# Optimization experiments

Measured on AMD Instinct MI355X. Metric: run time of the kernel, lower is better.

Reference implementation:

```python
import jax, jax.numpy as jnp
import numpy as np
import math

B, T, D_MOTION = 2, 1536, 256
D_MODEL, N_HEADS, D_FF, N_LAYERS = 512, 8, 2048, 6
D_HEAD = D_MODEL // N_HEADS
FPS = 30
PERIOD = FPS // 2
CONTEXT_FRAMES = 10
NEG = -1e9  # large negative instead of -inf so fully-masked rows give uniform attn, not NaN


def _w(k, shape, fan_in):
    return jax.random.normal(k, shape, jnp.float32) / np.sqrt(fan_in)


def setup_inputs() -> dict:
    key = jax.random.key(0)
    ks = jax.random.split(key, 16)
    L = N_LAYERS
    din = D_MOTION + 5 + 1
    inp = {
        'motion': jax.random.normal(ks[0], (B, T, D_MOTION), jnp.float32),
        'traj': jax.random.normal(ks[1], (B, T, 5), jnp.float32),
        'me_w1': _w(ks[2], (din, D_MODEL), din), 'me_b1': jnp.zeros((D_MODEL,), jnp.float32),
        'me_w2': _w(ks[3], (D_MODEL, D_MODEL), D_MODEL), 'me_b2': jnp.zeros((D_MODEL,), jnp.float32),
        'wq': _w(ks[4], (L, D_MODEL, D_MODEL), D_MODEL), 'bq': jnp.zeros((L, D_MODEL), jnp.float32),
        'wk': _w(ks[5], (L, D_MODEL, D_MODEL), D_MODEL), 'bk': jnp.zeros((L, D_MODEL), jnp.float32),
        'wv': _w(ks[6], (L, D_MODEL, D_MODEL), D_MODEL), 'bv': jnp.zeros((L, D_MODEL), jnp.float32),
        'wo': _w(ks[7], (L, D_MODEL, D_MODEL), D_MODEL), 'bo': jnp.zeros((L, D_MODEL), jnp.float32),
        'ln1_g': jnp.ones((L, D_MODEL), jnp.float32), 'ln1_b': jnp.zeros((L, D_MODEL), jnp.float32),
        'ffn_w1': _w(ks[8], (L, D_MODEL, D_FF), D_MODEL), 'ffn_b1': jnp.zeros((L, D_FF), jnp.float32),
        'ffn_w2': _w(ks[9], (L, D_FF, D_MODEL), D_FF), 'ffn_b2': jnp.zeros((L, D_MODEL), jnp.float32),
        'ln2_g': jnp.ones((L, D_MODEL), jnp.float32), 'ln2_b': jnp.zeros((L, D_MODEL), jnp.float32),
        'fln_g': jnp.ones((D_MODEL,), jnp.float32), 'fln_b': jnp.zeros((D_MODEL,), jnp.float32),
        'dec_w1': _w(ks[10], (D_MODEL, D_MODEL), D_MODEL), 'dec_b1': jnp.zeros((D_MODEL,), jnp.float32),
        'dec_w2': _w(ks[11], (D_MODEL, D_MOTION), D_MODEL), 'dec_b2': jnp.zeros((D_MOTION,), jnp.float32),
    }
    return inp


def _layer_norm(x, g, b):
    m = jnp.mean(x, axis=-1, keepdims=True)
    v = jnp.mean((x - m) ** 2, axis=-1, keepdims=True)
    return (x - m) * jax.lax.rsqrt(v + 1e-5) * g + b


def _leaky(x):
    return jnp.where(x >= 0, x, 0.01 * x)


def _forward(motion, traj, me_w1, me_b1, me_w2, me_b2, wq, bq, wk, bk, wv, bv, wo, bo,
             ln1_g, ln1_b, ffn_w1, ffn_b1, ffn_w2, ffn_b2, ln2_g, ln2_b,
             fln_g, fln_b, dec_w1, dec_b1, dec_w2, dec_b2):
    idx = jnp.arange(T)
    dist = jnp.abs(idx[:, None] - idx[None, :])                       # [T,T]
    atten_bias = -(dist // PERIOD).astype(jnp.float32)                # periodic distance bias

    # context mask: keep first context_frames and last frame
    batch_mask = jnp.ones((T, 1), jnp.float32).at[CONTEXT_FRAMES:-1].set(0.0)
    mask = jnp.broadcast_to(batch_mask[None], (B, T, 1))              # [B,T,1]
    cf = jnp.ones((T,), bool).at[CONTEXT_FRAMES:-1].set(False)        # constrained frames

    original_motion = motion
    motion = motion * mask

    # motion encoder (dropout inactive at eval)
    h = jnp.concatenate([motion, traj, mask], axis=-1)                # [B,T,D_MOTION+6]
    x = _leaky(h @ me_w1 + me_b1)
    x = _leaky(x @ me_w2 + me_b2)

    # periodic positional embedding (sinusoidal on pos mod period)
    pos = jnp.mod(jnp.arange(T, dtype=jnp.float32), float(PERIOD))
    half = D_MODEL // 2
    div = jnp.exp(-np.log(10000.0) * (2.0 * jnp.arange(half, dtype=jnp.float32)) / D_MODEL)
    ang = pos[:, None] * div[None, :]
    pe = jnp.concatenate([jnp.sin(ang), jnp.cos(ang)], axis=-1)       # [T,D_MODEL]
    x = x + pe[None]

    # dynamically growing attention window
    num_trans = T - CONTEXT_FRAMES - 1
    ksz = math.ceil(num_trans / 2 / N_LAYERS) * 2 + 1
    kern = jnp.ones((ksz,), jnp.float32)
    thr = ksz // 2
    scale = 1.0 / np.sqrt(D_HEAD)

    for i in range(N_LAYERS):
        # attn mask: True = blocked
        amask = (dist > thr) | (~cf)[None, :]                         # [T,T]
        h = _layer_norm(x, ln1_g[i], ln1_b[i])                        # pre-layernorm
        q = (h @ wq[i] + bq[i]).reshape(B, T, N_HEADS, D_HEAD)
        k = (h @ wk[i] + bk[i]).reshape(B, T, N_HEADS, D_HEAD)
        v = (h @ wv[i] + bv[i]).reshape(B, T, N_HEADS, D_HEAD)
        scores = jnp.einsum('bqhd,bkhd->bhqk', q, k) * scale + atten_bias
        scores = jnp.where(amask[None, None], NEG, scores)
        attn = jax.nn.softmax(scores, axis=-1)
        out = jnp.einsum('bhqk,bkhd->bqhd', attn, v).reshape(B, T, D_MODEL)
        x = x + out @ wo[i] + bo[i]
        # position-wise FFN (pre-layernorm)
        h = _layer_norm(x, ln2_g[i], ln2_b[i])
        x = x + jax.nn.relu(h @ ffn_w1[i] + ffn_b1[i]) @ ffn_w2[i] + ffn_b2[i]
        # grow constrained frames by conv1d with ones kernel (same padding)
        cf = jnp.convolve(cf.astype(jnp.float32), kern, mode='same') > 0.5

    x = _layer_norm(x, fln_g, fln_b)
    x = _leaky(x @ dec_w1 + dec_b1)
    x = x @ dec_w2 + dec_b2                                           # [B,T,D_MOTION]
    out = original_motion * mask + x * (1.0 - mask)
    return out, mask


def reference(motion, traj, me_w1, me_b1, me_w2, me_b2, wq, bq, wk, bk, wv, bv, wo, bo,
              ln1_g, ln1_b, ffn_w1, ffn_b1, ffn_w2, ffn_b2, ln2_g, ln2_b,
              fln_g, fln_b, dec_w1, dec_b1, dec_w2, dec_b2):
    return _forward(motion, traj, me_w1, me_b1, me_w2, me_b2, wq, bq, wk, bk, wv, bv, wo, bo,
                    ln1_g, ln1_b, ffn_w1, ffn_b1, ffn_w2, ffn_b2, ln2_g, ln2_b,
                    fln_g, fln_b, dec_w1, dec_b1, dec_w2, dec_b2)
```

## Files before the change

### kernel.cpp

```cpp
#include <hip/hip_runtime.h>
#include <math.h>

typedef unsigned short ushort_t;
typedef unsigned int uint_t;
typedef __bf16 bf16x4 __attribute__((ext_vector_type(4)));
typedef __bf16 bf16x8 __attribute__((ext_vector_type(8)));
typedef float f32x4 __attribute__((ext_vector_type(4)));

#define T_SEQ   1536
#define NB      2
#define MROWS   3072
#define DMODEL  512
#define NHEADS  8
#define DHEAD   64
#define DFF     2048
#define DMOTION 256
#define NLAYERS 6
#define PERIODN 15
#define CTXF    10
#define THRW    128
#define KIN     384

__device__ __forceinline__ float bf2f(ushort_t u) { return __uint_as_float((uint_t)u << 16); }
__device__ __forceinline__ ushort_t f2bf(float f) {
    uint_t x = __float_as_uint(f);
    return (ushort_t)((x + 0x7fffu + ((x >> 16) & 1u)) >> 16);
}

__device__ __forceinline__ void gl2lds(const ushort_t* g, ushort_t* l) {
    __builtin_amdgcn_global_load_lds((const __attribute__((address_space(1))) void*)g,
                                     (__attribute__((address_space(3))) void*)l, 16, 0, 0);
}

__global__ __launch_bounds__(256) void pe_k(float* __restrict__ pe) {
    int idx = blockIdx.x * 256 + threadIdx.x;
    if (idx >= PERIODN * DMODEL) return;
    int p = idx / DMODEL, c = idx % DMODEL;
    int j = (c < DMODEL / 2) ? c : (c - DMODEL / 2);
    float div = __expf(-logf(10000.0f) * (2.0f * (float)j) / (float)DMODEL);
    float ang = (float)p * div;
    pe[idx] = (c < DMODEL / 2) ? sinf(ang) : cosf(ang);
}

__global__ __launch_bounds__(256) void build_k(const float* __restrict__ motion,
                                               const float* __restrict__ traj,
                                               ushort_t* __restrict__ hin,
                                               float* __restrict__ mask_out) {
    int idx = blockIdx.x * 256 + threadIdx.x;
    if (idx >= MROWS * KIN) return;
    int row = idx / KIN, c = idx % KIN;
    int t = row % T_SEQ;
    float mv = (t < CTXF || t == T_SEQ - 1) ? 1.0f : 0.0f;
    float val;
    if (c < DMOTION)            val = motion[(size_t)row * DMOTION + c] * mv;
    else if (c < DMOTION + 5)   val = traj[(size_t)row * 5 + (c - DMOTION)];
    else if (c == DMOTION + 5)  val = mv;
    else                        val = 0.0f;
    hin[idx] = f2bf(val);
    if (c == 0) mask_out[row] = mv;
}

__global__ __launch_bounds__(256)
void tconv_k(const float* __restrict__ src, size_t sstride,
             ushort_t* __restrict__ dst, size_t dstride,
             int K, int N, int Kpad) {
    __shared__ float t[32][33];
    src += (size_t)blockIdx.z * sstride;
    dst += (size_t)blockIdx.z * dstride;
    const int kb = blockIdx.y * 32, nb = blockIdx.x * 32;
    const int tx = threadIdx.x & 31, ty = threadIdx.x >> 5;
#pragma unroll
    for (int i = 0; i < 4; ++i) {
        int k = kb + ty + i * 8, n = nb + tx;
        t[ty + i * 8][tx] = (k < K && n < N) ? src[(size_t)k * N + n] : 0.0f;
    }
    __syncthreads();
#pragma unroll
    for (int i = 0; i < 4; ++i) {
        int n = nb + ty + i * 8, kk = kb + tx;
        if (n < N && kk < Kpad) dst[(size_t)n * Kpad + kk] = f2bf(t[tx][ty + i * 8]);
    }
}

__global__ __launch_bounds__(256)
void tconv_qkv_k(const float* __restrict__ wq, const float* __restrict__ wk,
                 const float* __restrict__ wv, ushort_t* __restrict__ qkvt) {
    __shared__ float t[32][33];
    const int z = blockIdx.z, s = z % 3, l = z / 3;
    const float* src = (s == 0 ? wq : s == 1 ? wk : wv) + (size_t)l * DMODEL * DMODEL;
    ushort_t* dst = qkvt + (size_t)z * DMODEL * DMODEL;
    const int kb = blockIdx.y * 32, nb = blockIdx.x * 32;
    const int tx = threadIdx.x & 31, ty = threadIdx.x >> 5;
#pragma unroll
    for (int i = 0; i < 4; ++i)
        t[ty + i * 8][tx] = src[(size_t)(kb + ty + i * 8) * DMODEL + nb + tx];
    __syncthreads();
#pragma unroll
    for (int i = 0; i < 4; ++i)
        dst[(size_t)(nb + ty + i * 8) * DMODEL + kb + tx] = f2bf(t[tx][ty + i * 8]);
}

__global__ __launch_bounds__(256)
void bcat_k(const float* __restrict__ bq, const float* __restrict__ bk,
            const float* __restrict__ bv, float* __restrict__ bqkv) {
    int idx = blockIdx.x * 256 + threadIdx.x;
    if (idx >= NLAYERS * 3 * DMODEL) return;
    int l = idx / (3 * DMODEL), n = idx % (3 * DMODEL);
    int s = n >> 9, c = n & 511;
    const float* b = (s == 0 ? bq : s == 1 ? bk : bv);
    bqkv[idx] = b[l * DMODEL + c];
}

#define CL  68
template <int ACT, bool RES, bool PE, bool OUTBF>
__global__ __launch_bounds__(256)
void qgemm_k(const ushort_t* __restrict__ A, int K,
             const ushort_t* __restrict__ Wt,
             const float* __restrict__ bias,
             const float* __restrict__ res,
             const float* __restrict__ pe15,
             void* __restrict__ Cout, int N) {
    __shared__ ushort_t smem[2][(32 + 64) * 128];
    const int tid = threadIdx.x;
    const int lane = tid & 63, wid = tid >> 6;
    const int m0 = blockIdx.y * 32, n0 = blockIdx.x * 64;
    const int l4 = lane >> 4, l15 = lane & 15;
    const int lrow = lane >> 4;
    const int lu   = lane & 15;

    f32x4 acc[2][4];
#pragma unroll
    for (int m = 0; m < 2; ++m)
#pragma unroll
        for (int n = 0; n < 4; ++n) acc[m][n] = (f32x4){0.f, 0.f, 0.f, 0.f};

    const int niter = K >> 7;

    auto stage = [&](int buf, int k0) {
        ushort_t* dst = &smem[buf][0];
#pragma unroll
        for (int j = 0; j < 6; ++j) {
            const int inst = wid * 6 + j;
            if (inst < 8) {
                const int row = inst * 4 + lrow;
                const int u = lu ^ (row & 15);
                gl2lds(A + (size_t)(m0 + row) * K + k0 + u * 8, dst + inst * 512);
            } else {
                const int bi = inst - 8;
                const int row = bi * 4 + lrow;
                const int u = lu ^ (row & 15);
                gl2lds(Wt + (size_t)(n0 + row) * K + k0 + u * 8,
                       dst + 32 * 128 + bi * 512);
            }
        }
    };

    const int kbyte = wid * 64;
    auto rdfrag = [&](const ushort_t* t, int row) -> bf16x8 {
        const int off0 = kbyte + l4 * 8;
        const int off1 = kbyte + 32 + l4 * 8;
        const int a0 = row * 256 + (((off0 & ~15) ^ ((row & 15) << 4)) | (off0 & 15));
        const int a1 = row * 256 + (((off1 & ~15) ^ ((row & 15) << 4)) | (off1 & 15));
        bf16x4 lo = *(const bf16x4*)((const char*)t + a0);
        bf16x4 hi = *(const bf16x4*)((const char*)t + a1);
        return __builtin_shufflevector(lo, hi, 0, 1, 2, 3, 4, 5, 6, 7);
    };

    stage(0, 0);
    __syncthreads();
    int cur = 0;
    for (int t = 0; t < niter; ++t) {
        if (t + 1 < niter) stage(cur ^ 1, (t + 1) << 7);
        const ushort_t* As = &smem[cur][0];
        const ushort_t* Bs = &smem[cur][32 * 128];
        bf16x8 af[2], bf[4];
#pragma unroll
        for (int m = 0; m < 2; ++m) af[m] = rdfrag(As, m * 16 + l15);
#pragma unroll
        for (int n = 0; n < 4; ++n) bf[n] = rdfrag(Bs, n * 16 + l15);
#pragma unroll
        for (int m = 0; m < 2; ++m)
#pragma unroll
            for (int n = 0; n < 4; ++n)
                acc[m][n] = __builtin_amdgcn_mfma_f32_16x16x32_bf16(af[m], bf[n], acc[m][n], 0, 0, 0);
        __syncthreads();
        cur ^= 1;
    }

    float* cb0 = (float*)&smem[0][0];
    float* cb1 = (float*)&smem[1][0];
    if (wid >= 2) {
        float* cb = (wid == 2) ? cb0 : cb1;
#pragma unroll
        for (int m = 0; m < 2; ++m)
#pragma unroll
            for (int n = 0; n < 4; ++n)
#pragma unroll
                for (int r = 0; r < 4; ++r)
                    cb[(m * 16 + l4 * 4 + r) * CL + n * 16 + l15] = acc[m][n][r];
    }
    __syncthreads();
    if (wid < 2) {
        float* cb = (wid == 0) ? cb0 : cb1;
#pragma unroll
        for (int m = 0; m < 2; ++m)
#pragma unroll
            for (int n = 0; n < 4; ++n)
#pragma unroll
                for (int r = 0; r < 4; ++r)
                    cb[(m * 16 + l4 * 4 + r) * CL + n * 16 + l15] += acc[m][n][r];
    }
    __syncthreads();

    const int row = tid >> 3, c0 = (tid & 7) * 8;
    const int grow = m0 + row;
#pragma unroll
    for (int j = 0; j < 8; ++j) {
        const int gcol = n0 + c0 + j;
        float v = cb0[row * CL + c0 + j] + cb1[row * CL + c0 + j] + bias[gcol];
        if (ACT == 1) v = v >= 0.f ? v : 0.01f * v;
        else if (ACT == 2) v = fmaxf(v, 0.f);
        if (PE) v += pe15[((grow % T_SEQ) % PERIODN) * DMODEL + gcol];
        if (RES) v += res[(size_t)grow * N + gcol];
        if (OUTBF) ((ushort_t*)Cout)[(size_t)grow * N + gcol] = f2bf(v);
        else       ((float*)Cout)[(size_t)grow * N + gcol] = v;
    }
}

__global__ __launch_bounds__(256)
void ln_k(const float* __restrict__ X, const float* __restrict__ g,
          const float* __restrict__ b, ushort_t* __restrict__ Y) {
    const int wid = threadIdx.x >> 6, lane = threadIdx.x & 63;
    const int row = blockIdx.x * 4 + wid;
    const float* x = X + (size_t)row * DMODEL;
    float v[8], s = 0.f;
#pragma unroll
    for (int j = 0; j < 8; ++j) { v[j] = x[lane + 64 * j]; s += v[j]; }
#pragma unroll
    for (int o = 32; o; o >>= 1) s += __shfl_xor(s, o);
    const float mean = s * (1.0f / DMODEL);
    float vs = 0.f;
#pragma unroll
    for (int j = 0; j < 8; ++j) { float d = v[j] - mean; vs += d * d; }
#pragma unroll
    for (int o = 32; o; o >>= 1) vs += __shfl_xor(vs, o);
    const float inv = rsqrtf(vs * (1.0f / DMODEL) + 1e-5f);
    ushort_t* y = Y + (size_t)row * DMODEL;
#pragma unroll
    for (int j = 0; j < 8; ++j) {
        const int c = lane + 64 * j;
        y[c] = f2bf((v[j] - mean) * inv * g[c] + b[c]);
    }
}

__global__ __launch_bounds__(1024)
void vmeanp_k(const ushort_t* __restrict__ qkv, float* __restrict__ vmp) {
    __shared__ float red[16][64];
    const int bh = blockIdx.x, ch = blockIdx.y;
    const int b = bh >> 3, h = bh & 7;
    const int wid = threadIdx.x >> 6, lane = threadIdx.x & 63;
    const ushort_t* Vb = qkv + (size_t)(b * T_SEQ) * 1536 + 1024 + h * 64 + lane;
    float s = 0.f;
    const int t0 = ch * 192;
    for (int t = t0 + wid; t < t0 + 192; t += 16) s += bf2f(Vb[(size_t)t * 1536]);
    red[wid][lane] = s;
    __syncthreads();
    if (wid == 0) {
        float tot = 0.f;
#pragma unroll
        for (int i = 0; i < 16; ++i) tot += red[i][lane];
        vmp[(ch * 16 + bh) * 64 + lane] = tot;
    }
}

__global__ __launch_bounds__(1024)
void vmred_k(const float* __restrict__ vmp, float* __restrict__ vm) {
    const int t = threadIdx.x;
    float s = 0.f;
#pragma unroll
    for (int ch = 0; ch < 8; ++ch) s += vmp[ch * 1024 + t];
    vm[t] = s * (1.0f / T_SEQ);
}

__global__ __launch_bounds__(256)
void vfill_k(const float* __restrict__ vm, ushort_t* __restrict__ attout, int q0) {
    const int qrow = q0 + blockIdx.x, b = blockIdx.y;
    const int tid = threadIdx.x;
#pragma unroll
    for (int r = 0; r < 2; ++r) {
        const int c = tid + r * 256;
        attout[(size_t)(b * T_SEQ + qrow) * DMODEL + c] = f2bf(vm[b * 512 + c]);
    }
}

#define KLD 72
#define VLD 36
__global__ __launch_bounds__(256)
void attn3_k(const ushort_t* __restrict__ qkv, ushort_t* __restrict__ attout,
             int lo, int hi, int nlow, int qhi0, int tl, int st) {
    __shared__ ushort_t klds_[4][32 * KLD];
    __shared__ ushort_t vlds_[4][64 * VLD];
    const int lane = threadIdx.x & 63, wid = threadIdx.x >> 6;
    const int s = blockIdx.x * 4 + wid;
    if (s >= st) return;
    const int h = blockIdx.y, b = blockIdx.z;
    const int l15 = lane & 15, l4 = lane >> 4;

    int qb, qend;
    if (s < tl) { qb = 16 * s;                qend = nlow - 1; }
    else        { qb = qhi0 + 16 * (s - tl);  qend = T_SEQ - 1; }
    const int nr = qend - qb;

    ushort_t* klds = klds_[wid];
    ushort_t* vlds = vlds_[wid];
    const size_t rbase = (size_t)(b * T_SEQ) * 1536;
    const int q = qb + l15;

    const int qrow_r = min(q, T_SEQ - 1);
    const ushort_t* qptr = qkv + rbase + (size_t)qrow_r * 1536 + h * 64;
    bf16x8 bq[2];
#pragma unroll
    for (int kh = 0; kh < 2; ++kh) {
        bf16x4 lo4 = *(const bf16x4*)(qptr + kh * 32 + l4 * 4);
        bf16x4 hi4 = *(const bf16x4*)(qptr + kh * 32 + 16 + l4 * 4);
        bq[kh] = __builtin_shufflevector(lo4, hi4, 0, 1, 2, 3, 4, 5, 6, 7);
    }

    const int band0 = max(0, qb - THRW);
    const int band1 = min(T_SEQ - 1, qb + 15 + THRW);
    const int i1s = band0, i1e = min(band1, lo - 1);
    const int i2s = max(band0, hi), i2e = band1;

    f32x4 O[4] = {{0.f,0.f,0.f,0.f},{0.f,0.f,0.f,0.f},{0.f,0.f,0.f,0.f},{0.f,0.f,0.f,0.f}};
    float m = -3.0e38f, lsum = 0.f;

#pragma unroll 1
    for (int seg = 0; seg < 2; ++seg) {
        const int s0 = seg ? i2s : i1s, s1 = seg ? i2e : i1e;
#pragma unroll 1
        for (int c0 = s0; c0 <= s1; c0 += 32) {
#pragma unroll
            for (int i = 0; i < 4; ++i) {
                const int idx = i * 64 + lane;
                const int row = idx >> 3, c = (idx & 7) * 8;
                const int kr = min(c0 + row, T_SEQ - 1);
                const uint4 kv = *(const uint4*)(qkv + rbase + (size_t)kr * 1536 + 512 + h * 64 + c);
                *(uint4*)&klds[row * KLD + c] = kv;
                const uint4 vv = *(const uint4*)(qkv + rbase + (size_t)kr * 1536 + 1024 + h * 64 + c);
                const ushort_t* vp = (const ushort_t*)&vv;
#pragma unroll
                for (int d = 0; d < 8; ++d) vlds[(c + d) * VLD + row] = vp[d];
            }
            f32x4 sacc[2];
#pragma unroll
            for (int ks = 0; ks < 2; ++ks) {
                f32x4 a = {0.f, 0.f, 0.f, 0.f};
#pragma unroll
                for (int kh = 0; kh < 2; ++kh) {
                    const ushort_t* kp = &klds[(16 * ks + l15) * KLD + kh * 32];
                    bf16x4 lo4 = *(const bf16x4*)(kp + l4 * 4);
                    bf16x4 hi4 = *(const bf16x4*)(kp + 16 + l4 * 4);
                    bf16x8 ak = __builtin_shufflevector(lo4, hi4, 0, 1, 2, 3, 4, 5, 6, 7);
                    a = __builtin_amdgcn_mfma_f32_16x16x32_bf16(ak, bq[kh], a, 0, 0, 0);
                }
                sacc[ks] = a;
            }
            float sv[8];
            bool vld[8];
            float cm = -3.0e38f;
#pragma unroll
            for (int ks = 0; ks < 2; ++ks)
#pragma unroll
                for (int r = 0; r < 4; ++r) {
                    const int key = c0 + 16 * ks + 4 * l4 + r;
                    const int dist = (q > key) ? (q - key) : (key - q);
                    const bool v = (dist <= THRW) && (key < lo || key >= hi) && (key < T_SEQ);
                    const int ii = ks * 4 + r;
                    sv[ii] = sacc[ks][r] * 0.125f - (float)(dist / PERIODN);
                    vld[ii] = v;
                    cm = fmaxf(cm, v ? sv[ii] : -3.0e38f);
                }
            cm = fmaxf(cm, __shfl_xor(cm, 16));
            cm = fmaxf(cm, __shfl_xor(cm, 32));
            const float mnew = fmaxf(m, cm);
            const float sc = __expf(m - mnew);
            m = mnew;
            float p[8], psum = 0.f;
#pragma unroll
            for (int ii = 0; ii < 8; ++ii) {
                p[ii] = vld[ii] ? __expf(sv[ii] - mnew) : 0.f;
                psum += p[ii];
            }
            psum += __shfl_xor(psum, 16);
            psum += __shfl_xor(psum, 32);
            lsum = lsum * sc + psum;
#pragma unroll
            for (int ds = 0; ds < 4; ++ds) O[ds] *= sc;
            bf16x8 pb;
#pragma unroll
            for (int ii = 0; ii < 8; ++ii) pb[ii] = (__bf16)p[ii];
#pragma unroll
            for (int ds = 0; ds < 4; ++ds) {
                const ushort_t* vp2 = &vlds[(16 * ds + l15) * VLD];
                bf16x4 lo4 = *(const bf16x4*)(vp2 + 4 * l4);
                bf16x4 hi4 = *(const bf16x4*)(vp2 + 16 + 4 * l4);
                bf16x8 av = __builtin_shufflevector(lo4, hi4, 0, 1, 2, 3, 4, 5, 6, 7);
                O[ds] = __builtin_amdgcn_mfma_f32_16x16x32_bf16(av, pb, O[ds], 0, 0, 0);
            }
        }
    }
    if (l15 <= nr) {
        const float inv = 1.0f / lsum;
        ushort_t* op = attout + (size_t)(b * T_SEQ + qb + l15) * DMODEL + h * 64;
#pragma unroll
        for (int ds = 0; ds < 4; ++ds)
#pragma unroll
            for (int r = 0; r < 4; ++r)
                op[16 * ds + 4 * l4 + r] = f2bf(O[ds][r] * inv);
    }
}

__global__ __launch_bounds__(256)
void final_k(const float* __restrict__ motion, const float* __restrict__ xdec,
             float* __restrict__ out) {
    int idx = blockIdx.x * 256 + threadIdx.x;
    if (idx >= MROWS * DMOTION) return;
    const int row = idx >> 8;
    const int t = row % T_SEQ;
    const float mv = (t < CTXF || t == T_SEQ - 1) ? 1.0f : 0.0f;
    out[idx] = motion[idx] * mv + xdec[idx] * (1.0f - mv);
}

extern "C" void kernel_launch(void* const* d_in, const int* in_sizes, int n_in,
                              void* d_out, int out_size, void* d_ws, size_t ws_size,
                              hipStream_t stream) {
    const float* motion = (const float*)d_in[0];
    const float* traj   = (const float*)d_in[1];
    const float* me_w1  = (const float*)d_in[2];
    const float* me_b1  = (const float*)d_in[3];
    const float* me_w2  = (const float*)d_in[4];
    const float* me_b2  = (const float*)d_in[5];
    const float* wq = (const float*)d_in[6];
    const float* bq = (const float*)d_in[7];
    const float* wk = (const float*)d_in[8];
    const float* bk = (const float*)d_in[9];
    const float* wv = (const float*)d_in[10];
    const float* bv = (const float*)d_in[11];
    const float* wo = (const float*)d_in[12];
    const float* bo = (const float*)d_in[13];
    const float* ln1_g = (const float*)d_in[14];
    const float* ln1_b = (const float*)d_in[15];
    const float* ffn_w1 = (const float*)d_in[16];
    const float* ffn_b1 = (const float*)d_in[17];
    const float* ffn_w2 = (const float*)d_in[18];
    const float* ffn_b2 = (const float*)d_in[19];
    const float* ln2_g = (const float*)d_in[20];
    const float* ln2_b = (const float*)d_in[21];
    const float* fln_g = (const float*)d_in[22];
    const float* fln_b = (const float*)d_in[23];
    const float* dec_w1 = (const float*)d_in[24];
    const float* dec_b1 = (const float*)d_in[25];
    const float* dec_w2 = (const float*)d_in[26];
    const float* dec_b2 = (const float*)d_in[27];

    float* out = (float*)d_out;
    float* mask_out = out + (size_t)MROWS * DMOTION;

    char* base = (char*)d_ws;
    auto alloc = [&](size_t bytes) { char* p = base; base += (bytes + 255) & ~(size_t)255; return p; };

    ushort_t* qkvt  = (ushort_t*)alloc((size_t)NLAYERS * 1536 * 512 * 2);
    ushort_t* wot   = (ushort_t*)alloc((size_t)NLAYERS * 512 * 512 * 2);
    ushort_t* ffn1t = (ushort_t*)alloc((size_t)NLAYERS * 2048 * 512 * 2);
    ushort_t* ffn2t = (ushort_t*)alloc((size_t)NLAYERS * 512 * 2048 * 2);
    ushort_t* mew1t = (ushort_t*)alloc((size_t)512 * KIN * 2);
    ushort_t* mew2t = (ushort_t*)alloc((size_t)512 * 512 * 2);
    ushort_t* dec1t = (ushort_t*)alloc((size_t)512 * 512 * 2);
    ushort_t* dec2t = (ushort_t*)alloc((size_t)256 * 512 * 2);
    float*    bqkv  = (float*)alloc((size_t)NLAYERS * 1536 * 4);
    float*    pe15  = (float*)alloc((size_t)PERIODN * DMODEL * 4);
    float*    vmp   = (float*)alloc((size_t)8 * 16 * 64 * 4);
    float*    vm    = (float*)alloc((size_t)16 * 64 * 4);
    ushort_t* hin   = (ushort_t*)alloc((size_t)MROWS * KIN * 2);
    float*    x     = (float*)alloc((size_t)MROWS * DMODEL * 4);
    ushort_t* h     = (ushort_t*)alloc((size_t)MROWS * DMODEL * 2);
    ushort_t* qkv   = (ushort_t*)alloc((size_t)MROWS * 1536 * 2);
    ushort_t* ff    = (ushort_t*)alloc((size_t)MROWS * DFF * 2);
    float*    xdec  = (float*)qkv;

    const dim3 blk(256);
    pe_k<<<(PERIODN * DMODEL + 255) / 256, blk, 0, stream>>>(pe15);
    build_k<<<(MROWS * KIN + 255) / 256, blk, 0, stream>>>(motion, traj, hin, mask_out);

    tconv_qkv_k<<<dim3(16, 16, 18), blk, 0, stream>>>(wq, wk, wv, qkvt);
    tconv_k<<<dim3(16, 16, 6), blk, 0, stream>>>(wo, 512 * 512, wot, 512 * 512, 512, 512, 512);
    tconv_k<<<dim3(64, 16, 6), blk, 0, stream>>>(ffn_w1, 512 * 2048, ffn1t, 2048 * 512, 512, 2048, 512);
    tconv_k<<<dim3(16, 64, 6), blk, 0, stream>>>(ffn_w2, 2048 * 512, ffn2t, 512 * 2048, 2048, 512, 2048);
    tconv_k<<<dim3(16, 12, 1), blk, 0, stream>>>(me_w1, 0, mew1t, 0, 262, 512, KIN);
    tconv_k<<<dim3(16, 16, 1), blk, 0, stream>>>(me_w2, 0, mew2t, 0, 512, 512, 512);
    tconv_k<<<dim3(16, 16, 1), blk, 0, stream>>>(dec_w1, 0, dec1t, 0, 512, 512, 512);
    tconv_k<<<dim3(8, 16, 1),  blk, 0, stream>>>(dec_w2, 0, dec2t, 0, 512, 256, 512);
    bcat_k<<<(NLAYERS * 1536 + 255) / 256, blk, 0, stream>>>(bq, bk, bv, bqkv);

    const dim3 gs512(8, 96), gs1536(24, 96), gsff(32, 96), gs256(4, 96);

    qgemm_k<1, false, false, true ><<<gs512, blk, 0, stream>>>(hin, KIN, mew1t, me_b1, nullptr, nullptr, h, 512);
    qgemm_k<1, false, true,  false><<<gs512, blk, 0, stream>>>(h, 512, mew2t, me_b2, nullptr, pe15, x, 512);

    for (int i = 0; i < NLAYERS; ++i) {
        const int lo = CTXF + THRW * i;
        const int hi = (T_SEQ - 1) - THRW * i;
        int qlow_end = lo + 127;
        int qhi0 = hi - 128;
        int nlow, ninact;
        if (qhi0 <= qlow_end + 1) {
            nlow = T_SEQ; qhi0 = T_SEQ; ninact = 0;
        } else {
            nlow = qlow_end + 1;
            ninact = qhi0 - nlow;
        }
        const int tl2 = (nlow + 15) / 16;
        const int th2 = (T_SEQ - qhi0 + 15) / 16;
        const int st  = tl2 + th2;

        ln_k<<<MROWS / 4, blk, 0, stream>>>(x, ln1_g + i * 512, ln1_b + i * 512, h);
        qgemm_k<0, false, false, true><<<gs1536, blk, 0, stream>>>(h, 512, qkvt + (size_t)i * 1536 * 512, bqkv + i * 1536, nullptr, nullptr, qkv, 1536);
        if (ninact > 0) {
            vmeanp_k<<<dim3(16, 8), dim3(1024), 0, stream>>>(qkv, vmp);
            vmred_k<<<1, dim3(1024), 0, stream>>>(vmp, vm);
            vfill_k<<<dim3(ninact, NB), blk, 0, stream>>>(vm, h, nlow);
        }
        attn3_k<<<dim3((st + 3) / 4, NHEADS, NB), blk, 0, stream>>>(qkv, h, lo, hi, nlow, qhi0, tl2, st);
        qgemm_k<0, true, false, false><<<gs512, blk, 0, stream>>>(h, 512, wot + (size_t)i * 512 * 512, bo + i * 512, x, nullptr, x, 512);
        ln_k<<<MROWS / 4, blk, 0, stream>>>(x, ln2_g + i * 512, ln2_b + i * 512, h);
        qgemm_k<2, false, false, true><<<gsff, blk, 0, stream>>>(h, 512, ffn1t + (size_t)i * 2048 * 512, ffn_b1 + i * 2048, nullptr, nullptr, ff, 2048);
        qgemm_k<0, true, false, false><<<gs512, blk, 0, stream>>>(ff, 2048, ffn2t + (size_t)i * 512 * 2048, ffn_b2 + i * 512, x, nullptr, x, 512);
    }

    ln_k<<<MROWS / 4, blk, 0, stream>>>(x, fln_g, fln_b, h);
    qgemm_k<1, false, false, true ><<<gs512, blk, 0, stream>>>(h, 512, dec1t, dec_b1, nullptr, nullptr, ff, 512);
    qgemm_k<0, false, false, false><<<gs256, blk, 0, stream>>>(ff, 512, dec2t, dec_b2, nullptr, nullptr, xdec, 256);

    final_k<<<(MROWS * DMOTION + 255) / 256, blk, 0, stream>>>(motion, xdec, out);
}
```

Before: 813.4 us.

## Fuse mask blend into decoder GEMM, compute V-mean from LN output, merge fill into attention

The final mask blend is folded into the last decoder GEMM epilogue (new ACT==3), which removes final_k and the xdec round trip. The V mean for inactive rows is now computed as mean(h)·Wv + bv from the layernorm output via vsum_k and vdot_k, and the fill of inactive rows moves into spare waves of the attention kernel, replacing the separate vmred and vfill launches. MFMA sections in attention are wrapped with s_setprio to raise wave priority. The result is fewer launches and less strided reading, but the V-mean path now relies on linearity, which changes its rounding relative to the bf16 V values.

```diff
diff --git a/kernel.cpp b/kernel.cpp
--- a/kernel.cpp
+++ b/kernel.cpp
@@ -220,6 +220,11 @@
         float v = cb0[row * CL + c0 + j] + cb1[row * CL + c0 + j] + bias[gcol];
         if (ACT == 1) v = v >= 0.f ? v : 0.01f * v;
         else if (ACT == 2) v = fmaxf(v, 0.f);
+        else if (ACT == 3) {
+            const int t2 = grow % T_SEQ;
+            const float mv = (t2 < CTXF || t2 == T_SEQ - 1) ? 1.0f : 0.0f;
+            v = res[(size_t)grow * N + gcol] * mv + v * (1.0f - mv);
+        }
         if (PE) v += pe15[((grow % T_SEQ) % PERIODN) * DMODEL + gcol];
         if (RES) v += res[(size_t)grow * N + gcol];
         if (OUTBF) ((ushort_t*)Cout)[(size_t)grow * N + gcol] = f2bf(v);
@@ -254,56 +259,68 @@
 }
 
 __global__ __launch_bounds__(1024)
-void vmeanp_k(const ushort_t* __restrict__ qkv, float* __restrict__ vmp) {
-    __shared__ float red[16][64];
-    const int bh = blockIdx.x, ch = blockIdx.y;
-    const int b = bh >> 3, h = bh & 7;
-    const int wid = threadIdx.x >> 6, lane = threadIdx.x & 63;
-    const ushort_t* Vb = qkv + (size_t)(b * T_SEQ) * 1536 + 1024 + h * 64 + lane;
+void vsum_k(const ushort_t* __restrict__ h, float* __restrict__ hp) {
+    __shared__ float red[1024];
+    const int b = blockIdx.x, ch = blockIdx.y;
+    const int c = threadIdx.x & 511, half = threadIdx.x >> 9;
+    const ushort_t* hb = h + (size_t)(b * T_SEQ + ch * 192) * DMODEL + c;
     float s = 0.f;
-    const int t0 = ch * 192;
-    for (int t = t0 + wid; t < t0 + 192; t += 16) s += bf2f(Vb[(size_t)t * 1536]);
-    red[wid][lane] = s;
-    __syncthreads();
-    if (wid == 0) {
-        float tot = 0.f;
-#pragma unroll
-        for (int i = 0; i < 16; ++i) tot += red[i][lane];
-        vmp[(ch * 16 + bh) * 64 + lane] = tot;
-    }
-}
-
-__global__ __launch_bounds__(1024)
-void vmred_k(const float* __restrict__ vmp, float* __restrict__ vm) {
+    for (int r = half; r < 192; r += 2) s += bf2f(hb[(size_t)r * DMODEL]);
+    red[threadIdx.x] = s;
+    __syncthreads();
+    if (threadIdx.x < 512)
+        hp[(b * 8 + ch) * 512 + threadIdx.x] = red[threadIdx.x] + red[threadIdx.x + 512];
+}
+
+__global__ __launch_bounds__(256)
+void vdot_k(const float* __restrict__ hp, const ushort_t* __restrict__ wvt,
+            const float* __restrict__ bv, float* __restrict__ vm) {
+    __shared__ float mh[512];
+    __shared__ float red[256];
+    const int b = blockIdx.x, seg = blockIdx.y;
     const int t = threadIdx.x;
+    for (int c = t; c < 512; c += 256) {
+        float s = 0.f;
+#pragma unroll
+        for (int ch = 0; ch < 8; ++ch) s += hp[(b * 8 + ch) * 512 + c];
+        mh[c] = s * (1.0f / T_SEQ);
+    }
+    __syncthreads();
+    const int col = seg * 128 + (t & 127);
+    const int kh = (t >> 7) * 256;
+    const ushort_t* w = wvt + (size_t)col * 512 + kh;
     float s = 0.f;
-#pragma unroll
-    for (int ch = 0; ch < 8; ++ch) s += vmp[ch * 1024 + t];
-    vm[t] = s * (1.0f / T_SEQ);
-}
-
-__global__ __launch_bounds__(256)
-void vfill_k(const float* __restrict__ vm, ushort_t* __restrict__ attout, int q0) {
-    const int qrow = q0 + blockIdx.x, b = blockIdx.y;
-    const int tid = threadIdx.x;
-#pragma unroll
-    for (int r = 0; r < 2; ++r) {
-        const int c = tid + r * 256;
-        attout[(size_t)(b * T_SEQ + qrow) * DMODEL + c] = f2bf(vm[b * 512 + c]);
-    }
+    for (int k = 0; k < 256; k += 8) {
+        bf16x8 w8 = *(const bf16x8*)(w + k);
+#pragma unroll
+        for (int j = 0; j < 8; ++j) s += mh[kh + k + j] * (float)w8[j];
+    }
+    red[t] = s;
+    __syncthreads();
+    if (t < 128) vm[b * 512 + col] = red[t] + red[t + 128] + bv[col];
 }
 
 #define KLD 72
 #define VLD 36
 __global__ __launch_bounds__(256)
-void attn3_k(const ushort_t* __restrict__ qkv, ushort_t* __restrict__ attout,
-             int lo, int hi, int nlow, int qhi0, int tl, int st) {
+void attn3_k(const ushort_t* __restrict__ qkv, const float* __restrict__ vm,
+             ushort_t* __restrict__ attout,
+             int lo, int hi, int nlow, int qhi0, int tl, int st, int ft) {
     __shared__ ushort_t klds_[4][32 * KLD];
     __shared__ ushort_t vlds_[4][64 * VLD];
     const int lane = threadIdx.x & 63, wid = threadIdx.x >> 6;
     const int s = blockIdx.x * 4 + wid;
-    if (s >= st) return;
     const int h = blockIdx.y, b = blockIdx.z;
+    if (s >= st) {
+        const int f = s - st;
+        if (f >= ft) return;
+        const int r0 = nlow + 16 * f;
+        const int rend = min(16, qhi0 - r0);
+        const ushort_t ov = f2bf(vm[b * 512 + h * 64 + lane]);
+        ushort_t* op = attout + (size_t)(b * T_SEQ + r0) * DMODEL + h * 64 + lane;
+        for (int r = 0; r < rend; ++r) op[(size_t)r * DMODEL] = ov;
+        return;
+    }
     const int l15 = lane & 15, l4 = lane >> 4;
 
     int qb, qend;
@@ -352,6 +369,7 @@
                 for (int d = 0; d < 8; ++d) vlds[(c + d) * VLD + row] = vp[d];
             }
             f32x4 sacc[2];
+            __builtin_amdgcn_s_setprio(1);
 #pragma unroll
             for (int ks = 0; ks < 2; ++ks) {
                 f32x4 a = {0.f, 0.f, 0.f, 0.f};
@@ -365,6 +383,7 @@
                 }
                 sacc[ks] = a;
             }
+            __builtin_amdgcn_s_setprio(0);
             float sv[8];
             bool vld[8];
             float cm = -3.0e38f;
@@ -399,6 +418,7 @@
             bf16x8 pb;
 #pragma unroll
             for (int ii = 0; ii < 8; ++ii) pb[ii] = (__bf16)p[ii];
+            __builtin_amdgcn_s_setprio(1);
 #pragma unroll
             for (int ds = 0; ds < 4; ++ds) {
                 const ushort_t* vp2 = &vlds[(16 * ds + l15) * VLD];
@@ -407,6 +427,7 @@
                 bf16x8 av = __builtin_shufflevector(lo4, hi4, 0, 1, 2, 3, 4, 5, 6, 7);
                 O[ds] = __builtin_amdgcn_mfma_f32_16x16x32_bf16(av, pb, O[ds], 0, 0, 0);
             }
+            __builtin_amdgcn_s_setprio(0);
         }
     }
     if (l15 <= nr) {
@@ -418,17 +439,6 @@
             for (int r = 0; r < 4; ++r)
                 op[16 * ds + 4 * l4 + r] = f2bf(O[ds][r] * inv);
     }
-}
-
-__global__ __launch_bounds__(256)
-void final_k(const float* __restrict__ motion, const float* __restrict__ xdec,
-             float* __restrict__ out) {
-    int idx = blockIdx.x * 256 + threadIdx.x;
-    if (idx >= MROWS * DMOTION) return;
-    const int row = idx >> 8;
-    const int t = row % T_SEQ;
-    const float mv = (t < CTXF || t == T_SEQ - 1) ? 1.0f : 0.0f;
-    out[idx] = motion[idx] * mv + xdec[idx] * (1.0f - mv);
 }
 
 extern "C" void kernel_launch(void* const* d_in, const int* in_sizes, int n_in,
@@ -479,14 +489,13 @@
     ushort_t* dec2t = (ushort_t*)alloc((size_t)256 * 512 * 2);
     float*    bqkv  = (float*)alloc((size_t)NLAYERS * 1536 * 4);
     float*    pe15  = (float*)alloc((size_t)PERIODN * DMODEL * 4);
-    float*    vmp   = (float*)alloc((size_t)8 * 16 * 64 * 4);
-    float*    vm    = (float*)alloc((size_t)16 * 64 * 4);
+    float*    hp    = (float*)alloc((size_t)NB * 8 * 512 * 4);
+    float*    vm    = (float*)alloc((size_t)NB * 512 * 4);
     ushort_t* hin   = (ushort_t*)alloc((size_t)MROWS * KIN * 2);
     float*    x     = (float*)alloc((size_t)MROWS * DMODEL * 4);
     ushort_t* h     = (ushort_t*)alloc((size_t)MROWS * DMODEL * 2);
     ushort_t* qkv   = (ushort_t*)alloc((size_t)MROWS * 1536 * 2);
     ushort_t* ff    = (ushort_t*)alloc((size_t)MROWS * DFF * 2);
-    float*    xdec  = (float*)qkv;
 
     const dim3 blk(256);
     pe_k<<<(PERIODN * DMODEL + 255) / 256, blk, 0, stream>>>(pe15);
@@ -522,15 +531,15 @@
         const int tl2 = (nlow + 15) / 16;
         const int th2 = (T_SEQ - qhi0 + 15) / 16;
         const int st  = tl2 + th2;
+        const int ft  = (ninact + 15) / 16;
 
         ln_k<<<MROWS / 4, blk, 0, stream>>>(x, ln1_g + i * 512, ln1_b + i * 512, h);
         qgemm_k<0, false, false, true><<<gs1536, blk, 0, stream>>>(h, 512, qkvt + (size_t)i * 1536 * 512, bqkv + i * 1536, nullptr, nullptr, qkv, 1536);
         if (ninact > 0) {
-            vmeanp_k<<<dim3(16, 8), dim3(1024), 0, stream>>>(qkv, vmp);
-            vmred_k<<<1, dim3(1024), 0, stream>>>(vmp, vm);
-            vfill_k<<<dim3(ninact, NB), blk, 0, stream>>>(vm, h, nlow);
+            vsum_k<<<dim3(NB, 8), dim3(1024), 0, stream>>>(h, hp);
+            vdot_k<<<dim3(NB, 4), blk, 0, stream>>>(hp, qkvt + (size_t)i * 1536 * 512 + (size_t)1024 * 512, bqkv + i * 1536 + 1024, vm);
         }
-        attn3_k<<<dim3((st + 3) / 4, NHEADS, NB), blk, 0, stream>>>(qkv, h, lo, hi, nlow, qhi0, tl2, st);
+        attn3_k<<<dim3((st + ft + 3) / 4, NHEADS, NB), blk, 0, stream>>>(qkv, vm, h, lo, hi, nlow, qhi0, tl2, st, ft);
         qgemm_k<0, true, false, false><<<gs512, blk, 0, stream>>>(h, 512, wot + (size_t)i * 512 * 512, bo + i * 512, x, nullptr, x, 512);
         ln_k<<<MROWS / 4, blk, 0, stream>>>(x, ln2_g + i * 512, ln2_b + i * 512, h);
         qgemm_k<2, false, false, true><<<gsff, blk, 0, stream>>>(h, 512, ffn1t + (size_t)i * 2048 * 512, ffn_b1 + i * 2048, nullptr, nullptr, ff, 2048);
@@ -539,7 +548,5 @@
 
     ln_k<<<MROWS / 4, blk, 0, stream>>>(x, fln_g, fln_b, h);
     qgemm_k<1, false, false, true ><<<gs512, blk, 0, stream>>>(h, 512, dec1t, dec_b1, nullptr, nullptr, ff, 512);
-    qgemm_k<0, false, false, false><<<gs256, blk, 0, stream>>>(ff, 512, dec2t, dec_b2, nullptr, nullptr, xdec, 256);
-
-    final_k<<<(MROWS * DMOTION + 255) / 256, blk, 0, stream>>>(motion, xdec, out);
-}
+    qgemm_k<3, false, false, false><<<gs256, blk, 0, stream>>>(ff, 512, dec2t, dec_b2, motion, nullptr, out, 256);
+}
```

Measured after the change: 851.9 us. 1.05x slower.
